# Kernel optimization log

Hardware: AMD Instinct MI355X
Metric: run time of the kernel (lower is better)

The kernel has to match this reference:

```python
import jax, jax.numpy as jnp
import numpy as np

B, T, C, H = 4, 2048, 1024, 16
HS = C // H  # head size 64
LN_EPS = 1e-5


def setup_inputs() -> dict:
    key = jax.random.key(0)
    ks = jax.random.split(key, 14)
    s = lambda fan_in: 1.0 / np.sqrt(fan_in)
    return {
        "x": jax.random.normal(ks[0], (B, T, C), jnp.float32),
        # weights stored [in, out] (transposed vs torch nn.Linear) for y = x @ W + b
        "c_attn_w": jax.random.normal(ks[1], (C, 3 * C), jnp.float32) * s(C),
        "c_attn_b": jnp.zeros((3 * C,), jnp.float32),
        "c_proj_w": jax.random.normal(ks[2], (C, C), jnp.float32) * s(C),
        "c_proj_b": jnp.zeros((C,), jnp.float32),
        "fc_w": jax.random.normal(ks[3], (C, 4 * C), jnp.float32) * s(C),
        "fc_b": jnp.zeros((4 * C,), jnp.float32),
        "proj_w": jax.random.normal(ks[4], (4 * C, C), jnp.float32) * s(4 * C),
        "proj_b": jnp.zeros((C,), jnp.float32),
        "ln1_g": jnp.ones((C,), jnp.float32),
        "ln1_b": jnp.zeros((C,), jnp.float32),
        "ln2_g": jnp.ones((C,), jnp.float32),
        "ln2_b": jnp.zeros((C,), jnp.float32),
    }


def layer_norm(x, g, b):
    mu = jnp.mean(x, axis=-1, keepdims=True)
    var = jnp.var(x, axis=-1, keepdims=True)
    return (x - mu) * jax.lax.rsqrt(var + LN_EPS) * g + b


def attention(x, c_attn_w, c_attn_b, c_proj_w, c_proj_b):
    Bs, Ts, Cs = x.shape
    qkv = x @ c_attn_w + c_attn_b  # (B,T,3C)
    q, k, v = jnp.split(qkv, 3, axis=-1)
    q = q.reshape(Bs, Ts, H, HS).transpose(0, 2, 1, 3)  # (B,H,T,hs)
    k = k.reshape(Bs, Ts, H, HS).transpose(0, 2, 1, 3)
    v = v.reshape(Bs, Ts, H, HS).transpose(0, 2, 1, 3)
    wei = jnp.einsum("bhqd,bhkd->bhqk", q, k) * (1.0 / np.sqrt(HS))
    causal = jnp.tril(jnp.ones((Ts, Ts), bool))
    wei = jnp.where(causal, wei, -jnp.inf)
    wei = jax.nn.softmax(wei, axis=-1)
    out = jnp.einsum("bhqk,bhkd->bhqd", wei, v)
    out = out.transpose(0, 2, 1, 3).reshape(Bs, Ts, Cs)
    return out @ c_proj_w + c_proj_b


def mlp(x, fc_w, fc_b, proj_w, proj_b):
    h = jax.nn.gelu(x @ fc_w + fc_b, approximate=True)
    return h @ proj_w + proj_b


def reference(x, c_attn_w, c_attn_b, c_proj_w, c_proj_b, fc_w, fc_b, proj_w, proj_b, ln1_g, ln1_b, ln2_g, ln2_b):
    x = x + attention(layer_norm(x, ln1_g, ln1_b), c_attn_w, c_attn_b, c_proj_w, c_proj_b)
    out = x + mlp(layer_norm(x, ln2_g, ln2_b), fc_w, fc_b, proj_w, proj_b)
    return out
```

## Files before the change

### kernel.cpp

```cpp
#include <hip/hip_runtime.h>

typedef unsigned short u16;
typedef __attribute__((ext_vector_type(8))) short bf16x8;
typedef __attribute__((ext_vector_type(4))) float f32x4;

#define SC_LOG2E 0.18033688011112043f
#define MB_LOG2E 17.31234049066756f

__device__ __forceinline__ float b2f(u16 u) {
  union { unsigned int i; float f; } v; v.i = ((unsigned int)u) << 16; return v.f;
}
__device__ __forceinline__ u16 f2b(float f) {
  unsigned int x = __float_as_uint(f);
  unsigned int r = (x + 0x7fffu + ((x >> 16) & 1u)) >> 16;
  return (u16)r;
}

#define GLOAD_LDS16(g, l)                                                              \
  __builtin_amdgcn_global_load_lds((const __attribute__((address_space(1))) void*)(g), \
                                   (__attribute__((address_space(3))) void*)(l), 16, 0, 0)

__global__ __launch_bounds__(256) void transpose_cast_kernel(const float* __restrict__ in,
                                                             u16* __restrict__ out,
                                                             int K, int N) {
  __shared__ float tile[64][65];
  const int tid = threadIdx.x;
  const int n0 = blockIdx.x * 64, k0 = blockIdx.y * 64;
#pragma unroll
  for (int it = 0; it < 4; ++it) {
    int lin = it * 256 + tid;
    int r = lin >> 4, c4 = (lin & 15) * 4;
    float4 v = *(const float4*)&in[(size_t)(k0 + r) * N + n0 + c4];
    tile[r][c4 + 0] = v.x; tile[r][c4 + 1] = v.y;
    tile[r][c4 + 2] = v.z; tile[r][c4 + 3] = v.w;
  }
  __syncthreads();
#pragma unroll
  for (int it = 0; it < 2; ++it) {
    int lin = it * 256 + tid;
    int r = lin >> 3, c8 = (lin & 7) * 8;
    u16 tmp[8];
#pragma unroll
    for (int j = 0; j < 8; ++j) tmp[j] = f2b(tile[c8 + j][r]);
    *(uint4*)&out[(size_t)(n0 + r) * K + k0 + c8] = *(const uint4*)tmp;
  }
}

__global__ __launch_bounds__(256) void transpose_v_kernel(const u16* __restrict__ qkv,
                                                          u16* __restrict__ vt) {
  __shared__ float tl[64][65];
  const int tid = threadIdx.x;
  const int bh = blockIdx.y, b = bh >> 4, h = bh & 15;
  const int t0 = blockIdx.x * 64;
  const int voff = 2048 + h * 64;
#pragma unroll
  for (int it = 0; it < 2; ++it) {
    int lin = it * 256 + tid;
    int tt = lin >> 3, d8 = (lin & 7) * 8;
    uint4 v = *(const uint4*)&qkv[((size_t)b * 2048 + t0 + tt) * 3072 + voff + d8];
    const u16* p = (const u16*)&v;
#pragma unroll
    for (int j = 0; j < 8; ++j) tl[tt][d8 + j] = b2f(p[j]);
  }
  __syncthreads();
#pragma unroll
  for (int it = 0; it < 2; ++it) {
    int lin = it * 256 + tid;
    int d = lin >> 3, t8 = (lin & 7) * 8;
    u16 tmp[8];
#pragma unroll
    for (int j = 0; j < 8; ++j) tmp[j] = f2b(tl[t8 + j][d]);
    *(uint4*)&vt[((size_t)bh * 64 + d) * 2048 + t0 + t8] = *(const uint4*)tmp;
  }
}

template <bool INF32>
__global__ __launch_bounds__(256) void ln_kernel(const void* __restrict__ xv,
                                                 const float* __restrict__ g,
                                                 const float* __restrict__ b,
                                                 u16* __restrict__ o, int C) {
  const int row = blockIdx.x, tid = threadIdx.x;
  const int wave = tid >> 6, lane = tid & 63;
  const int base = tid * 4;
  float f[4];
  if (INF32) {
    float4 v = *(const float4*)((const float*)xv + (size_t)row * C + base);
    f[0] = v.x; f[1] = v.y; f[2] = v.z; f[3] = v.w;
  } else {
    ushort4 v = *(const ushort4*)((const u16*)xv + (size_t)row * C + base);
    f[0] = b2f(v.x); f[1] = b2f(v.y); f[2] = b2f(v.z); f[3] = b2f(v.w);
  }
  float s = f[0] + f[1] + f[2] + f[3];
  float q = f[0] * f[0] + f[1] * f[1] + f[2] * f[2] + f[3] * f[3];
#pragma unroll
  for (int off = 1; off < 64; off <<= 1) {
    s += __shfl_xor(s, off);
    q += __shfl_xor(q, off);
  }
  __shared__ float reds[4], redq[4];
  if (lane == 0) { reds[wave] = s; redq[wave] = q; }
  __syncthreads();
  float S = reds[0] + reds[1] + reds[2] + reds[3];
  float Q = redq[0] + redq[1] + redq[2] + redq[3];
  const float inv = 1.0f / (float)C;
  float mean = S * inv;
  float var = Q * inv - mean * mean;
  float rs = rsqrtf(var + 1e-5f);
  float4 gv = *(const float4*)&g[base];
  float4 bv = *(const float4*)&b[base];
  ushort4 ov;
  ov.x = f2b((f[0] - mean) * rs * gv.x + bv.x);
  ov.y = f2b((f[1] - mean) * rs * gv.y + bv.y);
  ov.z = f2b((f[2] - mean) * rs * gv.z + bv.z);
  ov.w = f2b((f[3] - mean) * rs * gv.w + bv.w);
  *(ushort4*)&o[(size_t)row * C + base] = ov;
}

__device__ __forceinline__ float gelu_fn(float v) {
  float c = v + 0.044715f * v * v * v;
  return 0.5f * v * (1.0f + tanhf(0.7978845608028654f * c));
}

template <bool GELU, int RESMODE, bool OUTF32>
__global__ __launch_bounds__(256) void gemm_kernel(const u16* __restrict__ A,
                                                   const u16* __restrict__ Bt,
                                                   const float* __restrict__ bias,
                                                   const void* __restrict__ res,
                                                   void* __restrict__ Cv,
                                                   int M, int N, int K) {
  __shared__ u16 As[128 * 64];
  __shared__ u16 Bs[128 * 64];
  const int tid = threadIdx.x;
  const int wave = tid >> 6, lane = tid & 63;
  const int lhi = lane >> 4, llo = lane & 15;
  const int sw = llo & 7;
  const int m0 = blockIdx.x * 128, n0 = blockIdx.y * 128;
  const int wr = (wave >> 1) * 64, wc = (wave & 1) * 64;

  f32x4 acc[4][4] = {};

  for (int k0 = 0; k0 < K; k0 += 64) {
#pragma unroll
    for (int p = 0; p < 4; ++p) {
      int s = p * 256 + tid;
      int r = s >> 3;
      int c = ((s & 7) ^ (r & 7)) * 8;
      GLOAD_LDS16(A + (size_t)(m0 + r) * K + k0 + c, As + s * 8);
      GLOAD_LDS16(Bt + (size_t)(n0 + r) * K + k0 + c, Bs + s * 8);
    }
    __syncthreads();
#pragma unroll
    for (int kk = 0; kk < 2; ++kk) {
      const int cp = ((kk * 4 + lhi) ^ sw) * 8;
      bf16x8 af[4], bf[4];
#pragma unroll
      for (int i = 0; i < 4; ++i)
        af[i] = *(const bf16x8*)&As[(wr + i * 16 + llo) * 64 + cp];
#pragma unroll
      for (int j = 0; j < 4; ++j)
        bf[j] = *(const bf16x8*)&Bs[(wc + j * 16 + llo) * 64 + cp];
#pragma unroll
      for (int i = 0; i < 4; ++i)
#pragma unroll
        for (int j = 0; j < 4; ++j)
          acc[i][j] = __builtin_amdgcn_mfma_f32_16x16x32_bf16(af[i], bf[j], acc[i][j], 0, 0, 0);
    }
    __syncthreads();
  }

#pragma unroll
  for (int i = 0; i < 4; ++i) {
    int row = m0 + wr + i * 16 + lhi * 4;
#pragma unroll
    for (int j = 0; j < 4; ++j) {
      int col = n0 + wc + j * 16 + llo;
      float bv = bias[col];
#pragma unroll
      for (int r = 0; r < 4; ++r) {
        float v = acc[i][j][r] + bv;
        if (GELU) v = gelu_fn(v);
        size_t idx = (size_t)(row + r) * N + col;
        if (RESMODE == 1) v += b2f(((const u16*)res)[idx]);
        if (RESMODE == 2) v += ((const float*)res)[idx];
        if (OUTF32) ((float*)Cv)[idx] = v;
        else ((u16*)Cv)[idx] = f2b(v);
      }
    }
  }
}

__global__ __launch_bounds__(256) void attn_kernel(const u16* __restrict__ qkv,
                                                   const u16* __restrict__ vt,
                                                   u16* __restrict__ out) {
  __shared__ u16 Ks[64 * 68];
  __shared__ u16 Vs[64 * 68];
  __shared__ u16 Ps[128 * 68];
  const int tid = threadIdx.x;
  const int wave = tid >> 6, lane = tid & 63;
  const int lhi = lane >> 4, llo = lane & 15;
  const int pr = blockIdx.x;
  const int bh = blockIdx.y;
  const int b = bh >> 4, h = bh & 15;
  const size_t rowbase = (size_t)b * 2048;
  const int qoff = h * 64, koff = 1024 + h * 64;
  const u16* vtb = vt + (size_t)bh * 64 * 2048;
  const int sr = tid >> 3;
  const int sc = (tid & 7) * 8;

#pragma unroll
  for (int ph = 0; ph < 2; ++ph) {
    const int qtile = ph ? pr : (15 - pr);
    const int q0 = qtile * 128;

    bf16x8 qf[2][2];
#pragma unroll
    for (int t = 0; t < 2; ++t)
#pragma unroll
      for (int kk = 0; kk < 2; ++kk) {
        uint4 v = *(const uint4*)&qkv[(rowbase + q0 + t * 64 + wave * 16 + llo) * 3072 +
                                      qoff + kk * 32 + lhi * 8];
        qf[t][kk] = *(const bf16x8*)&v;
      }

    f32x4 oacc[2][4] = {};
    float l_st[2][4] = {};
    const int qr0[2] = {q0 + wave * 16, q0 + 64 + wave * 16};
    const int nkt = 2 * qtile + 2;

    uint4 pk[2], pv[2];
#pragma unroll
    for (int it = 0; it < 2; ++it) {
      int r = it * 32 + sr;
      pk[it] = *(const uint4*)&qkv[(rowbase + r) * 3072 + koff + sc];
      pv[it] = *(const uint4*)&vtb[(size_t)r * 2048 + sc];
    }

    for (int kt = 0; kt < nkt; ++kt) {
      const int kt0 = kt * 64;
      __syncthreads();
#pragma unroll
      for (int it = 0; it < 2; ++it) {
        int r = it * 32 + sr;
        *(uint4*)&Ks[r * 68 + sc] = pk[it];
        *(uint4*)&Vs[r * 68 + sc] = pv[it];
      }
      __syncthreads();
      if (kt + 1 < nkt) {
        const int nt0 = kt0 + 64;
#pragma unroll
        for (int it = 0; it < 2; ++it) {
          int r = it * 32 + sr;
          pk[it] = *(const uint4*)&qkv[(rowbase + nt0 + r) * 3072 + koff + sc];
          pv[it] = *(const uint4*)&vtb[(size_t)r * 2048 + nt0 + sc];
        }
      }

      const bool act0 = (kt0 <= qr0[0] + 15);

      f32x4 s[2][4] = {};
#pragma unroll
      for (int kk = 0; kk < 2; ++kk)
#pragma unroll
        for (int j = 0; j < 4; ++j) {
          bf16x8 kf = *(const bf16x8*)&Ks[(j * 16 + llo) * 68 + kk * 32 + lhi * 8];
          s[0][j] = __builtin_amdgcn_mfma_f32_16x16x32_bf16(qf[0][kk], kf, s[0][j], 0, 0, 0);
          s[1][j] = __builtin_amdgcn_mfma_f32_16x16x32_bf16(qf[1][kk], kf, s[1][j], 0, 0, 0);
        }

#pragma unroll
      for (int t = 0; t < 2; ++t) {
        if (t == 0 && !act0) continue;
        const int q_base = qr0[t];
        const bool msk = (kt0 + 63 > q_base);
        u16* psrow = &Ps[(wave * 32 + t * 16) * 68];
#pragma unroll
        for (int j = 0; j < 4; ++j) {
          const int key = kt0 + j * 16 + llo;
#pragma unroll
          for (int r = 0; r < 4; ++r) {
            float sv = s[t][j][r];
            if (msk) sv = (key <= q_base + lhi * 4 + r) ? sv : -1e30f;
            float p = __builtin_amdgcn_exp2f(__builtin_fmaf(sv, SC_LOG2E, -MB_LOG2E));
            l_st[t][r] += p;
            psrow[(lhi * 4 + r) * 68 + j * 16 + llo] = (u16)(__float_as_uint(p) >> 16);
          }
        }
      }

#pragma unroll
      for (int kc = 0; kc < 2; ++kc) {
        bf16x8 pf0 = *(const bf16x8*)&Ps[(wave * 32 + llo) * 68 + kc * 32 + lhi * 8];
        bf16x8 pf1 = *(const bf16x8*)&Ps[(wave * 32 + 16 + llo) * 68 + kc * 32 + lhi * 8];
#pragma unroll
        for (int j4 = 0; j4 < 4; ++j4) {
          bf16x8 vf = *(const bf16x8*)&Vs[(j4 * 16 + llo) * 68 + kc * 32 + lhi * 8];
          if (act0) oacc[0][j4] = __builtin_amdgcn_mfma_f32_16x16x32_bf16(pf0, vf, oacc[0][j4], 0, 0, 0);
          oacc[1][j4] = __builtin_amdgcn_mfma_f32_16x16x32_bf16(pf1, vf, oacc[1][j4], 0, 0, 0);
        }
      }
    }

#pragma unroll
    for (int t = 0; t < 2; ++t)
#pragma unroll
      for (int r = 0; r < 4; ++r) {
        float v = l_st[t][r];
        v += __shfl_xor(v, 1);
        v += __shfl_xor(v, 2);
        v += __shfl_xor(v, 4);
        v += __shfl_xor(v, 8);
        l_st[t][r] = 1.0f / v;
      }
#pragma unroll
    for (int t = 0; t < 2; ++t)
#pragma unroll
      for (int j4 = 0; j4 < 4; ++j4)
#pragma unroll
        for (int r = 0; r < 4; ++r) {
          size_t row = rowbase + q0 + t * 64 + wave * 16 + lhi * 4 + r;
          out[row * 1024 + h * 64 + j4 * 16 + llo] = f2b(oacc[t][j4][r] * l_st[t][r]);
        }
  }
}

extern "C" void kernel_launch(void* const* d_in, const int* in_sizes, int n_in,
                              void* d_out, int out_size, void* d_ws, size_t ws_size,
                              hipStream_t stream) {
  const float* x        = (const float*)d_in[0];
  const float* c_attn_w = (const float*)d_in[1];
  const float* c_attn_b = (const float*)d_in[2];
  const float* c_proj_w = (const float*)d_in[3];
  const float* c_proj_b = (const float*)d_in[4];
  const float* fc_w     = (const float*)d_in[5];
  const float* fc_b     = (const float*)d_in[6];
  const float* proj_w   = (const float*)d_in[7];
  const float* proj_b   = (const float*)d_in[8];
  const float* ln1_g    = (const float*)d_in[9];
  const float* ln1_b    = (const float*)d_in[10];
  const float* ln2_g    = (const float*)d_in[11];
  const float* ln2_b    = (const float*)d_in[12];
  float* out = (float*)d_out;
  u16* ws = (u16*)d_ws;

  const size_t M = 8192;
  u16* ln_buf = ws;
  u16* qkv    = ln_buf + M * 1024;
  u16* x1     = qkv + M * 3072;
  u16* hbuf   = x1 + M * 1024;
  u16* wT_a   = hbuf + M * 4096;
  u16* wT_p   = wT_a + 3072 * 1024;
  u16* wT_f   = wT_p + 1024 * 1024;
  u16* wT_m   = wT_f + 4096 * 1024;
  u16* vt     = hbuf;

  dim3 blk(256);
  transpose_cast_kernel<<<dim3(48, 16), blk, 0, stream>>>(c_attn_w, wT_a, 1024, 3072);
  transpose_cast_kernel<<<dim3(16, 16), blk, 0, stream>>>(c_proj_w, wT_p, 1024, 1024);
  transpose_cast_kernel<<<dim3(64, 16), blk, 0, stream>>>(fc_w, wT_f, 1024, 4096);
  transpose_cast_kernel<<<dim3(16, 64), blk, 0, stream>>>(proj_w, wT_m, 4096, 1024);

  ln_kernel<true><<<8192, blk, 0, stream>>>(x, ln1_g, ln1_b, ln_buf, 1024);
  gemm_kernel<false, 0, false><<<dim3(64, 24), blk, 0, stream>>>(ln_buf, wT_a, c_attn_b, nullptr, qkv, 8192, 3072, 1024);
  transpose_v_kernel<<<dim3(32, 64), blk, 0, stream>>>(qkv, vt);
  attn_kernel<<<dim3(8, 64), blk, 0, stream>>>(qkv, vt, ln_buf);
  gemm_kernel<false, 2, false><<<dim3(64, 8), blk, 0, stream>>>(ln_buf, wT_p, c_proj_b, x, x1, 8192, 1024, 1024);
  ln_kernel<false><<<8192, blk, 0, stream>>>(x1, ln2_g, ln2_b, ln_buf, 1024);
  gemm_kernel<true, 0, false><<<dim3(64, 32), blk, 0, stream>>>(ln_buf, wT_f, fc_b, nullptr, hbuf, 8192, 4096, 1024);
  gemm_kernel<false, 1, true><<<dim3(64, 8), blk, 0, stream>>>(hbuf, wT_m, proj_b, x1, out, 8192, 1024, 4096);
}
```

Baseline: 548.5 us.

## Split attention keys three ways across blocks and add a combine kernel

The attention grid gains a third dimension of size 3. Each block handles every third key tile with double-buffered K/V shared memory and writes unnormalised partial outputs and row sums to scratch buffers, and a new combine kernel adds the partials and normalises. This raises block count from 512 to 1536 to improve GPU occupancy, at the cost of extra partial-output traffic, bf16 rounding of the partials and one more launch. Separately, GELU's tanh is replaced by an exp2/rcp formulation to cut epilogue cost in the FC GEMM.

Result: no change. 549.5 us (+0.2%).

```diff
diff --git a/kernel.cpp b/kernel.cpp
--- a/kernel.cpp
+++ b/kernel.cpp
@@ -117,8 +117,11 @@
 }
 
 __device__ __forceinline__ float gelu_fn(float v) {
-  float c = v + 0.044715f * v * v * v;
-  return 0.5f * v * (1.0f + tanhf(0.7978845608028654f * c));
+  float v2 = v * v;
+  float u = v * __builtin_fmaf(0.035677408136300125f, v2, 0.7978845608028654f);
+  float a = fminf(u * 2.885390081777927f, 80.0f);
+  float E = __builtin_amdgcn_exp2f(a);
+  return v * E * __builtin_amdgcn_rcpf(E + 1.0f);
 }
 
 template <bool GELU, int RESMODE, bool OUTF32>
@@ -191,19 +194,25 @@
 
 __global__ __launch_bounds__(256) void attn_kernel(const u16* __restrict__ qkv,
                                                    const u16* __restrict__ vt,
-                                                   u16* __restrict__ out) {
-  __shared__ u16 Ks[64 * 68];
-  __shared__ u16 Vs[64 * 68];
+                                                   u16* __restrict__ op0,
+                                                   u16* __restrict__ op1,
+                                                   u16* __restrict__ op2,
+                                                   float* __restrict__ lpart) {
+  __shared__ u16 Ks[2][64 * 68];
+  __shared__ u16 Vs[2][64 * 68];
   __shared__ u16 Ps[128 * 68];
   const int tid = threadIdx.x;
   const int wave = tid >> 6, lane = tid & 63;
   const int lhi = lane >> 4, llo = lane & 15;
   const int pr = blockIdx.x;
   const int bh = blockIdx.y;
+  const int sk = blockIdx.z;
   const int b = bh >> 4, h = bh & 15;
   const size_t rowbase = (size_t)b * 2048;
   const int qoff = h * 64, koff = 1024 + h * 64;
   const u16* vtb = vt + (size_t)bh * 64 * 2048;
+  u16* opart = (sk == 0) ? op0 : ((sk == 1) ? op1 : op2);
+  float* lp = lpart + sk * 131072 + bh * 2048;
   const int sr = tid >> 3;
   const int sc = (tid & 7) * 8;
 
@@ -211,6 +220,7 @@
   for (int ph = 0; ph < 2; ++ph) {
     const int qtile = ph ? pr : (15 - pr);
     const int q0 = qtile * 128;
+    const int nkt = 2 * qtile + 2;
 
     bf16x8 qf[2][2];
 #pragma unroll
@@ -225,28 +235,31 @@
     f32x4 oacc[2][4] = {};
     float l_st[2][4] = {};
     const int qr0[2] = {q0 + wave * 16, q0 + 64 + wave * 16};
-    const int nkt = 2 * qtile + 2;
+
+    __syncthreads();
 
     uint4 pk[2], pv[2];
-#pragma unroll
-    for (int it = 0; it < 2; ++it) {
-      int r = it * 32 + sr;
-      pk[it] = *(const uint4*)&qkv[(rowbase + r) * 3072 + koff + sc];
-      pv[it] = *(const uint4*)&vtb[(size_t)r * 2048 + sc];
-    }
-
-    for (int kt = 0; kt < nkt; ++kt) {
-      const int kt0 = kt * 64;
-      __syncthreads();
+    if (sk < nkt) {
 #pragma unroll
       for (int it = 0; it < 2; ++it) {
         int r = it * 32 + sr;
-        *(uint4*)&Ks[r * 68 + sc] = pk[it];
-        *(uint4*)&Vs[r * 68 + sc] = pv[it];
+        pk[it] = *(const uint4*)&qkv[(rowbase + sk * 64 + r) * 3072 + koff + sc];
+        pv[it] = *(const uint4*)&vtb[(size_t)r * 2048 + sk * 64 + sc];
+      }
+    }
+
+    int p = 0;
+    for (int kt = sk; kt < nkt; kt += 3, p ^= 1) {
+      const int kt0 = kt * 64;
+#pragma unroll
+      for (int it = 0; it < 2; ++it) {
+        int r = it * 32 + sr;
+        *(uint4*)&Ks[p][r * 68 + sc] = pk[it];
+        *(uint4*)&Vs[p][r * 68 + sc] = pv[it];
       }
       __syncthreads();
-      if (kt + 1 < nkt) {
-        const int nt0 = kt0 + 64;
+      if (kt + 3 < nkt) {
+        const int nt0 = kt0 + 192;
 #pragma unroll
         for (int it = 0; it < 2; ++it) {
           int r = it * 32 + sr;
@@ -262,7 +275,7 @@
       for (int kk = 0; kk < 2; ++kk)
 #pragma unroll
         for (int j = 0; j < 4; ++j) {
-          bf16x8 kf = *(const bf16x8*)&Ks[(j * 16 + llo) * 68 + kk * 32 + lhi * 8];
+          bf16x8 kf = *(const bf16x8*)&Ks[p][(j * 16 + llo) * 68 + kk * 32 + lhi * 8];
           s[0][j] = __builtin_amdgcn_mfma_f32_16x16x32_bf16(qf[0][kk], kf, s[0][j], 0, 0, 0);
           s[1][j] = __builtin_amdgcn_mfma_f32_16x16x32_bf16(qf[1][kk], kf, s[1][j], 0, 0, 0);
         }
@@ -280,9 +293,9 @@
           for (int r = 0; r < 4; ++r) {
             float sv = s[t][j][r];
             if (msk) sv = (key <= q_base + lhi * 4 + r) ? sv : -1e30f;
-            float p = __builtin_amdgcn_exp2f(__builtin_fmaf(sv, SC_LOG2E, -MB_LOG2E));
-            l_st[t][r] += p;
-            psrow[(lhi * 4 + r) * 68 + j * 16 + llo] = (u16)(__float_as_uint(p) >> 16);
+            float pp = __builtin_amdgcn_exp2f(__builtin_fmaf(sv, SC_LOG2E, -MB_LOG2E));
+            l_st[t][r] += pp;
+            psrow[(lhi * 4 + r) * 68 + j * 16 + llo] = (u16)(__float_as_uint(pp) >> 16);
           }
         }
       }
@@ -293,7 +306,7 @@
         bf16x8 pf1 = *(const bf16x8*)&Ps[(wave * 32 + 16 + llo) * 68 + kc * 32 + lhi * 8];
 #pragma unroll
         for (int j4 = 0; j4 < 4; ++j4) {
-          bf16x8 vf = *(const bf16x8*)&Vs[(j4 * 16 + llo) * 68 + kc * 32 + lhi * 8];
+          bf16x8 vf = *(const bf16x8*)&Vs[p][(j4 * 16 + llo) * 68 + kc * 32 + lhi * 8];
           if (act0) oacc[0][j4] = __builtin_amdgcn_mfma_f32_16x16x32_bf16(pf0, vf, oacc[0][j4], 0, 0, 0);
           oacc[1][j4] = __builtin_amdgcn_mfma_f32_16x16x32_bf16(pf1, vf, oacc[1][j4], 0, 0, 0);
         }
@@ -309,8 +322,15 @@
         v += __shfl_xor(v, 2);
         v += __shfl_xor(v, 4);
         v += __shfl_xor(v, 8);
-        l_st[t][r] = 1.0f / v;
-      }
+        l_st[t][r] = v;
+      }
+    if (llo == 0) {
+#pragma unroll
+      for (int t = 0; t < 2; ++t)
+#pragma unroll
+        for (int r = 0; r < 4; ++r)
+          lp[q0 + t * 64 + wave * 16 + lhi * 4 + r] = l_st[t][r];
+    }
 #pragma unroll
     for (int t = 0; t < 2; ++t)
 #pragma unroll
@@ -318,9 +338,32 @@
 #pragma unroll
         for (int r = 0; r < 4; ++r) {
           size_t row = rowbase + q0 + t * 64 + wave * 16 + lhi * 4 + r;
-          out[row * 1024 + h * 64 + j4 * 16 + llo] = f2b(oacc[t][j4][r] * l_st[t][r]);
+          opart[row * 1024 + h * 64 + j4 * 16 + llo] = f2b(oacc[t][j4][r]);
         }
   }
+}
+
+__global__ __launch_bounds__(256) void attn_combine_kernel(const u16* __restrict__ o0,
+                                                           const u16* __restrict__ o1,
+                                                           const u16* __restrict__ o2,
+                                                           const float* __restrict__ lp,
+                                                           u16* __restrict__ out) {
+  const int row = blockIdx.x;
+  const int b = row >> 11, t = row & 2047;
+  const int col = threadIdx.x * 4;
+  const int bh = b * 16 + (col >> 6);
+  const float l = lp[bh * 2048 + t] + lp[131072 + bh * 2048 + t] + lp[262144 + bh * 2048 + t];
+  const float rl = 1.0f / l;
+  const size_t base = (size_t)row * 1024 + col;
+  ushort4 a = *(const ushort4*)&o0[base];
+  ushort4 c = *(const ushort4*)&o1[base];
+  ushort4 d = *(const ushort4*)&o2[base];
+  ushort4 ov;
+  ov.x = f2b((b2f(a.x) + b2f(c.x) + b2f(d.x)) * rl);
+  ov.y = f2b((b2f(a.y) + b2f(c.y) + b2f(d.y)) * rl);
+  ov.z = f2b((b2f(a.z) + b2f(c.z) + b2f(d.z)) * rl);
+  ov.w = f2b((b2f(a.w) + b2f(c.w) + b2f(d.w)) * rl);
+  *(ushort4*)&out[base] = ov;
 }
 
 extern "C" void kernel_launch(void* const* d_in, const int* in_sizes, int n_in,
@@ -352,6 +395,8 @@
   u16* wT_f   = wT_p + 1024 * 1024;
   u16* wT_m   = wT_f + 4096 * 1024;
   u16* vt     = hbuf;
+  u16* opart2 = hbuf + 8388608;
+  float* lpart = (float*)(hbuf + 16777216);
 
   dim3 blk(256);
   transpose_cast_kernel<<<dim3(48, 16), blk, 0, stream>>>(c_attn_w, wT_a, 1024, 3072);
@@ -362,7 +407,8 @@
   ln_kernel<true><<<8192, blk, 0, stream>>>(x, ln1_g, ln1_b, ln_buf, 1024);
   gemm_kernel<false, 0, false><<<dim3(64, 24), blk, 0, stream>>>(ln_buf, wT_a, c_attn_b, nullptr, qkv, 8192, 3072, 1024);
   transpose_v_kernel<<<dim3(32, 64), blk, 0, stream>>>(qkv, vt);
-  attn_kernel<<<dim3(8, 64), blk, 0, stream>>>(qkv, vt, ln_buf);
+  attn_kernel<<<dim3(8, 64, 3), blk, 0, stream>>>(qkv, vt, ln_buf, x1, opart2, lpart);
+  attn_combine_kernel<<<8192, blk, 0, stream>>>(ln_buf, x1, opart2, lpart, ln_buf);
   gemm_kernel<false, 2, false><<<dim3(64, 8), blk, 0, stream>>>(ln_buf, wT_p, c_proj_b, x, x1, 8192, 1024, 1024);
   ln_kernel<false><<<8192, blk, 0, stream>>>(x1, ln2_g, ln2_b, ln_buf, 1024);
   gemm_kernel<true, 0, false><<<dim3(64, 32), blk, 0, stream>>>(ln_buf, wT_f, fc_b, nullptr, hbuf, 8192, 4096, 1024);
```
